# Optimization experiments

Measured on AMD Instinct MI355X. Metric: run time of the kernel, lower is better.

Reference implementation:

```python
import jax, jax.numpy as jnp
import numpy as np

B, CIN, COUT, N = 8, 64, 64, 4096
MODES, L, M = 64, 100, 20


def _cc_nodes_weights(m):
    # Clenshaw-Curtis nodes cos(k*pi/n) and weights on [-1, 1]
    n = m - 1
    k = np.arange(m)
    nodes = np.cos(np.pi * k / n)
    v = np.ones(m)
    for j in range(1, n // 2 + 1):
        b = 1.0 if 2 * j == n else 2.0
        v -= b / (4.0 * j * j - 1.0) * np.cos(2.0 * j * k * np.pi / n)
    w = 2.0 * v / n
    w[0] *= 0.5
    w[-1] *= 0.5
    return nodes, w


def setup_inputs() -> dict:
    key = jax.random.key(0)
    k1, k2, k3 = jax.random.split(key, 3)
    scale = 1.0 / (CIN * COUT)
    x = jax.random.normal(k1, (B, CIN, N), dtype=jnp.float32)
    w_real = scale * jax.random.uniform(k2, (CIN, COUT, MODES), dtype=jnp.float32)
    w_imag = scale * jax.random.uniform(k3, (CIN, COUT, MODES), dtype=jnp.float32)
    return {"x": x, "w_real": w_real, "w_imag": w_imag}


def _forward(x, w_real, w_imag):
    b, c, n = x.shape
    t = jnp.linspace(0.0, 1.0, n)
    f = np.fft.fftfreq(n, d=1.0 / n).astype(np.float32)  # integer freqs, fft order
    nodes, cw = _cc_nodes_weights(M)

    # ---- CFT: X(f) = sum_{segments l, cheb nodes k} w_lk * x(t_lk) * exp(-2i*pi*f*t_lk)
    h = 0.5 / L                               # segment half-width on [0,1]
    cents = (np.arange(L) + 0.5) / L
    t_nodes = (cents[:, None] + h * nodes[None, :]).ravel().astype(np.float32)  # (L*M,)
    wts = np.broadcast_to(h * cw, (L, M)).ravel().astype(np.float32)            # (L*M,)
    tq = jnp.asarray(t_nodes)
    # interpolate each (b, c) signal onto the Chebyshev quadrature nodes
    xs = jax.vmap(lambda s: jnp.interp(tq, t, s))(x.reshape(b * c, n))  # (BC, LM)
    phase = -2.0 * jnp.pi * jnp.asarray(f)[:, None] * tq[None, :]       # (N, LM)
    E = jnp.exp(1j * phase).astype(jnp.complex64) * jnp.asarray(wts)[None, :]
    x_cft = (xs.astype(jnp.complex64) @ E.T).reshape(b, c, n)           # (B, Cin, N)

    # ---- spectral channel mixing on lowest MODES fft-order frequencies
    w = (w_real + 1j * w_imag).astype(jnp.complex64)
    out_low = jnp.einsum('bix,iox->box', x_cft[:, :, :MODES], w)
    out_ft = jnp.concatenate(
        [out_low, jnp.zeros((b, COUT, n - MODES), dtype=jnp.complex64)], axis=-1)

    # ---- ICFT: x(t) = int X(f) exp(+2i*pi*f*t) df via the same segment quadrature
    order = np.argsort(f)
    f_sorted = f[order]
    cs = out_ft[:, :, jnp.asarray(order)].reshape(b * COUT, n)
    fa, fb = float(f_sorted[0]), float(f_sorted[-1])
    hf = (fb - fa) / (2.0 * L)
    fc = fa + (np.arange(L) + 0.5) * (fb - fa) / L
    f_nodes = (fc[:, None] + hf * nodes[None, :]).ravel().astype(np.float32)
    wfs = np.broadcast_to(hf * cw, (L, M)).ravel().astype(np.float32)
    fq = jnp.asarray(f_nodes)
    fs = jnp.asarray(f_sorted)
    ci = jax.vmap(lambda cv: jnp.interp(fq, fs, cv.real)
                  + 1j * jnp.interp(fq, fs, cv.imag))(cs)               # (BC, LM)
    phase2 = 2.0 * jnp.pi * fq[:, None] * t[None, :]                     # (LM, N)
    E2 = jnp.exp(1j * phase2).astype(jnp.complex64) * jnp.asarray(wfs)[:, None]
    return (ci.astype(jnp.complex64) @ E2).real.reshape(b, COUT, n)


def reference(x, w_real, w_imag):
    return _forward(x, w_real, w_imag)
```

## Files before the change

### kernel.cpp

```cpp
#include <hip/hip_runtime.h>


#define NN 4096
#define C1_19 0.9863613034027223
#define NS3 33
#define NSP 40

#define OFF_XRE 0
#define OFF_XIM 32768
#define OFF_Z   131072

__device__ __forceinline__ float sin_rev(float r) { return __builtin_amdgcn_sinf(r); }
__device__ __forceinline__ float cos_rev(float r) { return __builtin_amdgcn_cosf(r); }

__device__ __forceinline__ void build_tables(double* nd, double* cwd, int t) {
    if (t == 0) {
        nd[0] = 1.0; nd[1] = C1_19;
        for (int k = 2; k < 20; ++k) nd[k] = 2.0 * C1_19 * nd[k - 1] - nd[k - 2];
    }
    __syncthreads();
    if (t < 20) {
        double v = 1.0;
        for (int j = 1; j <= 9; ++j) {
            int q = (2 * j * t) % 38; if (q > 19) q = 38 - q;
            v -= 2.0 / (4.0 * j * j - 1.0) * nd[q];
        }
        double w = 2.0 * v / 19.0;
        if (t == 0 || t == 19) w *= 0.5;
        cwd[t] = w;
    }
}

__global__ __launch_bounds__(256) void k_cft(const float* __restrict__ x,
                                             float* __restrict__ ws) {
    __shared__ double nd[20], cwd[20];
    __shared__ __align__(16) float xs[2052];
    __shared__ __align__(16) float xq[1000];
    __shared__ __align__(16) float Fri[20][64][2];
    __shared__ float red[4][64][2];
    const int t = threadIdx.x;
    const int bc = blockIdx.x, h = blockIdx.y;
    const int i0 = h ? 2044 : 0;
    build_tables(nd, cwd, t);
    for (int idx = t; idx < 513; idx += 256)
        *(float4*)&xs[idx * 4] = *(const float4*)&x[(size_t)bc * NN + i0 + idx * 4];
    __syncthreads();
    for (int idx = t; idx < 1280; idx += 256) {
        int k = idx >> 6, m = idx & 63;
        double r = -0.005 * nd[k] * (double)m;
        r -= floor(r);
        float fr = (float)r;
        float w = (float)(0.005 * cwd[k]);
        Fri[k][m][0] = w * cos_rev(fr);
        Fri[k][m][1] = w * sin_rev(fr);
    }
    for (int idx = t; idx < 1000; idx += 256) {
        int l_loc = idx / 20, k = idx - l_loc * 20;
        int l = h * 50 + l_loc;
        double tq = 0.005 * ((double)(2 * l + 1) + nd[k]);
        double sf = tq * 4095.0;
        int i = (int)sf; if (i > 4094) i = 4094;
        double a = sf - (double)i;
        if (a < 0.0) a = 0.0; if (a > 1.0) a = 1.0;
        float af = (float)a;
        xq[idx] = (1.f - af) * xs[i - i0] + af * xs[i - i0 + 1];
    }
    __syncthreads();
    const int m = t & 63, grp = t >> 6;
    float Fre[20], Fim[20];
#pragma unroll
    for (int k = 0; k < 20; ++k) {
        Fre[k] = Fri[k][m][0];
        Fim[k] = Fri[k][m][1];
    }
    float ar = 0.f, ai = 0.f;
    for (int l_loc = grp; l_loc < 50; l_loc += 4) {
        const float4* q4 = (const float4*)&xq[l_loc * 20];
        float ur = 0.f, ui = 0.f;
#pragma unroll
        for (int c = 0; c < 5; ++c) {
            float4 q = q4[c];
            ur += q.x * Fre[c * 4]     + q.y * Fre[c * 4 + 1]
                + q.z * Fre[c * 4 + 2] + q.w * Fre[c * 4 + 3];
            ui += q.x * Fim[c * 4]     + q.y * Fim[c * 4 + 1]
                + q.z * Fim[c * 4 + 2] + q.w * Fim[c * 4 + 3];
        }
        int l = h * 50 + l_loc;
        int u = (m * (2 * l + 1)) % 200;
        float fr = (float)u * 0.005f;
        float tr = cos_rev(fr), ti = -sin_rev(fr);
        ar += tr * ur - ti * ui;
        ai += tr * ui + ti * ur;
    }
    red[grp][m][0] = ar;
    red[grp][m][1] = ai;
    __syncthreads();
    if (t < 64) {
        float sr = (red[0][t][0] + red[1][t][0]) + (red[2][t][0] + red[3][t][0]);
        float si = (red[0][t][1] + red[1][t][1]) + (red[2][t][1] + red[3][t][1]);
        const int base = h * 65536;
        ws[base + OFF_XRE + (size_t)bc * 64 + t] = sr;
        ws[base + OFF_XIM + (size_t)bc * 64 + t] = si;
    }
}

__global__ __launch_bounds__(256) void k_mix(const float* __restrict__ wr,
                                             const float* __restrict__ wi,
                                             float* __restrict__ ws) {
    __shared__ double nd[20], cwd[20];
    __shared__ float part[4][2][64];
    __shared__ float yt[2][64];
    __shared__ float sw0[NS3], sw1[NS3];
    __shared__ int   si0[NS3], si1[NS3];
    const int t = threadIdx.x;
    const int b = blockIdx.x >> 6, o = blockIdx.x & 63;
    build_tables(nd, cwd, t);
    __syncthreads();
    if (t < NS3) {
        int l = (t < 2) ? 49 : (t < 22 ? 50 : 51);
        int k = (t < 2) ? t : (t < 22 ? t - 2 : t - 13);
        double fq = -2048.0 + ((double)l + 0.5) * 40.95 + 20.475 * nd[k];
        int m0 = (int)floor(fq);
        float fr = (float)(fq - (double)m0);
        sw0[t] = (m0 >= 0 && m0 <= 63) ? (1.f - fr) : 0.f;
        sw1[t] = (m0 + 1 >= 0 && m0 + 1 <= 63) ? fr : 0.f;
        si0[t] = min(max(m0, 0), 63);
        si1[t] = min(max(m0 + 1, 0), 63);
    }
    const int m = t & 63, grp = t >> 6;
    float yr = 0.f, yi = 0.f;
#pragma unroll 4
    for (int i = grp * 16; i < grp * 16 + 16; ++i) {
        const size_t off = (size_t)(b * 64 + i) * 64 + m;
        float xr = ws[OFF_XRE + off] + ws[65536 + OFF_XRE + off];
        float xi = ws[OFF_XIM + off] + ws[65536 + OFF_XIM + off];
        float a = wr[((size_t)i * 64 + o) * 64 + m];
        float c = wi[((size_t)i * 64 + o) * 64 + m];
        yr += xr * a - xi * c;
        yi += xr * c + xi * a;
    }
    part[grp][0][m] = yr;
    part[grp][1][m] = yi;
    __syncthreads();
    if (t < 128) {
        int pr = t >> 6, mm = t & 63;
        yt[pr][mm] = ((part[0][pr][mm] + part[1][pr][mm]) +
                      (part[2][pr][mm] + part[3][pr][mm]));
    }
    __syncthreads();
    if (t < 2 * NS3) {
        int p = t >= NS3, s = t - p * NS3;
        float z = sw0[s] * yt[p][si0[s]] + sw1[s] * yt[p][si1[s]];
        ws[OFF_Z + (size_t)p * 512 * NSP + ((size_t)b * 64 + o) * NSP + s] = z;
    } else if (t < 2 * NS3 + 14) {
        int q = t - 2 * NS3;
        int p = q / 7, s = NS3 + q % 7;
        ws[OFF_Z + (size_t)p * 512 * NSP + ((size_t)b * 64 + o) * NSP + s] = 0.f;
    }
}

__global__ __launch_bounds__(256) void k_icft(const float* __restrict__ ws,
                                              float* __restrict__ out) {
    __shared__ double nd[20], cwd[20];
    __shared__ double sfq[NS3];
    __shared__ float  swf[NS3];
    __shared__ __align__(16) float zt[2][64][41];
    __shared__ __align__(16) float e2[2][NSP][36];
    const int t = threadIdx.x;
    const int jt2 = blockIdx.x, pc = blockIdx.y;
    build_tables(nd, cwd, t);
    __syncthreads();
    if (t < NS3) {
        int l = (t < 2) ? 49 : (t < 22 ? 50 : 51);
        int k = (t < 2) ? t : (t < 22 ? t - 2 : t - 13);
        sfq[t] = -2048.0 + ((double)l + 0.5) * 40.95 + 20.475 * nd[k];
        swf[t] = (float)(20.475 * cwd[k]);
    }
    for (int idx = t; idx < 2 * 64 * NSP; idx += 256) {
        int part = idx / (64 * NSP), rem = idx % (64 * NSP);
        int row = rem / NSP, s = rem % NSP;
        zt[part][row][s] =
            ws[OFF_Z + (size_t)part * 512 * NSP + ((size_t)pc * 64 + row) * NSP + s];
    }
    __syncthreads();
    const double inv4095 = 1.0 / 4095.0;
    for (int idx = t; idx < NSP * 32; idx += 256) {
        int s = idx >> 5, jl = idx & 31;
        float cr = 0.f, ci = 0.f;
        if (s < NS3) {
            double ph = sfq[s] * ((double)(jt2 * 32 + jl) * inv4095);
            ph -= floor(ph);
            float fr = (float)ph;
            cr = swf[s] * cos_rev(fr);
            ci = swf[s] * sin_rev(fr);
        }
        e2[0][s][jl + (jl >> 3) * 0] = cr;
        e2[1][s][jl] = ci;
        e2[0][s][jl] = cr;
    }
    __syncthreads();
    const int jg = t & 7, pg = t >> 3;
    float acc[2][4] = {{0.f}};
    for (int s0 = 0; s0 < NSP; s0 += 8) {
        float zr[2][8], zi[2][8];
#pragma unroll
        for (int p = 0; p < 2; ++p)
#pragma unroll
            for (int v = 0; v < 8; ++v) {
                zr[p][v] = zt[0][pg * 2 + p][s0 + v];
                zi[p][v] = zt[1][pg * 2 + p][s0 + v];
            }
#pragma unroll
        for (int v = 0; v < 8; ++v) {
            const float4 er = *(const float4*)&e2[0][s0 + v][jg * 4];
            const float4 ei = *(const float4*)&e2[1][s0 + v][jg * 4];
#pragma unroll
            for (int p = 0; p < 2; ++p) {
                acc[p][0] += zr[p][v] * er.x - zi[p][v] * ei.x;
                acc[p][1] += zr[p][v] * er.y - zi[p][v] * ei.y;
                acc[p][2] += zr[p][v] * er.z - zi[p][v] * ei.z;
                acc[p][3] += zr[p][v] * er.w - zi[p][v] * ei.w;
            }
        }
    }
#pragma unroll
    for (int p = 0; p < 2; ++p) {
        float4 r;
        r.x = acc[p][0]; r.y = acc[p][1]; r.z = acc[p][2]; r.w = acc[p][3];
        *(float4*)&out[(size_t)(pc * 64 + pg * 2 + p) * NN + jt2 * 32 + jg * 4] = r;
    }
}

extern "C" void kernel_launch(void* const* d_in, const int* in_sizes, int n_in,
                              void* d_out, int out_size, void* d_ws, size_t ws_size,
                              hipStream_t stream) {
    const float* x  = (const float*)d_in[0];
    const float* wr = (const float*)d_in[1];
    const float* wi = (const float*)d_in[2];
    float* out = (float*)d_out;
    float* ws  = (float*)d_ws;
    (void)in_sizes; (void)n_in; (void)out_size; (void)ws_size;

    k_cft<<<dim3(512, 2), 256, 0, stream>>>(x, ws);
    k_mix<<<512, 256, 0, stream>>>(wr, wi, ws);
    k_icft<<<dim3(128, 8), 256, 0, stream>>>(ws, out);
}
```

Measured before the change: 31.17 us.

## Fuse CFT and mode-mixing kernels using flag-based inter-block dependency

Merges the CFT and channel-mixing launches into one grid. The first 512 blocks each compute a full signal's CFT, with no split into halves. The remaining 512 blocks stage the weight slices in shared memory and spin-wait on per-row magic flags written into the output buffer before mixing. This removes one kernel launch, the half-split partial-sum round trip, and some strided global weight reads. In exchange it relies on producer blocks being scheduled before or alongside consumers to avoid deadlock, and it temporarily uses the output buffer as flag storage.

```diff
diff --git a/kernel.cpp b/kernel.cpp
--- a/kernel.cpp
+++ b/kernel.cpp
@@ -5,10 +5,11 @@
 #define C1_19 0.9863613034027223
 #define NS3 33
 #define NSP 40
+#define MAGIC 0x7fc0deadu
 
 #define OFF_XRE 0
 #define OFF_XIM 32768
-#define OFF_Z   131072
+#define OFF_Z   65536
 
 __device__ __forceinline__ float sin_rev(float r) { return __builtin_amdgcn_sinf(r); }
 __device__ __forceinline__ float cos_rev(float r) { return __builtin_amdgcn_cosf(r); }
@@ -31,131 +32,157 @@
     }
 }
 
-__global__ __launch_bounds__(256) void k_cft(const float* __restrict__ x,
-                                             float* __restrict__ ws) {
+struct PA { float xs[NN]; float xq[2000]; float Fri[20][64][2]; float red[4][64][2]; };
+struct PB { float wsl[2][64][64]; float part[4][2][64]; float yt[2][64]; };
+union SU { PA a; PB b; };
+
+__global__ __launch_bounds__(256, 4) void k_cftmix(const float* __restrict__ x,
+                                                   const float* __restrict__ wr,
+                                                   const float* __restrict__ wi,
+                                                   float* __restrict__ ws,
+                                                   float* __restrict__ out) {
+    __shared__ SU su;
     __shared__ double nd[20], cwd[20];
-    __shared__ __align__(16) float xs[2052];
-    __shared__ __align__(16) float xq[1000];
-    __shared__ __align__(16) float Fri[20][64][2];
-    __shared__ float red[4][64][2];
-    const int t = threadIdx.x;
-    const int bc = blockIdx.x, h = blockIdx.y;
-    const int i0 = h ? 2044 : 0;
-    build_tables(nd, cwd, t);
-    for (int idx = t; idx < 513; idx += 256)
-        *(float4*)&xs[idx * 4] = *(const float4*)&x[(size_t)bc * NN + i0 + idx * 4];
-    __syncthreads();
-    for (int idx = t; idx < 1280; idx += 256) {
-        int k = idx >> 6, m = idx & 63;
-        double r = -0.005 * nd[k] * (double)m;
-        r -= floor(r);
-        float fr = (float)r;
-        float w = (float)(0.005 * cwd[k]);
-        Fri[k][m][0] = w * cos_rev(fr);
-        Fri[k][m][1] = w * sin_rev(fr);
-    }
-    for (int idx = t; idx < 1000; idx += 256) {
-        int l_loc = idx / 20, k = idx - l_loc * 20;
-        int l = h * 50 + l_loc;
-        double tq = 0.005 * ((double)(2 * l + 1) + nd[k]);
-        double sf = tq * 4095.0;
-        int i = (int)sf; if (i > 4094) i = 4094;
-        double a = sf - (double)i;
-        if (a < 0.0) a = 0.0; if (a > 1.0) a = 1.0;
-        float af = (float)a;
-        xq[idx] = (1.f - af) * xs[i - i0] + af * xs[i - i0 + 1];
-    }
-    __syncthreads();
-    const int m = t & 63, grp = t >> 6;
-    float Fre[20], Fim[20];
-#pragma unroll
-    for (int k = 0; k < 20; ++k) {
-        Fre[k] = Fri[k][m][0];
-        Fim[k] = Fri[k][m][1];
-    }
-    float ar = 0.f, ai = 0.f;
-    for (int l_loc = grp; l_loc < 50; l_loc += 4) {
-        const float4* q4 = (const float4*)&xq[l_loc * 20];
-        float ur = 0.f, ui = 0.f;
-#pragma unroll
-        for (int c = 0; c < 5; ++c) {
-            float4 q = q4[c];
-            ur += q.x * Fre[c * 4]     + q.y * Fre[c * 4 + 1]
-                + q.z * Fre[c * 4 + 2] + q.w * Fre[c * 4 + 3];
-            ui += q.x * Fim[c * 4]     + q.y * Fim[c * 4 + 1]
-                + q.z * Fim[c * 4 + 2] + q.w * Fim[c * 4 + 3];
-        }
-        int l = h * 50 + l_loc;
-        int u = (m * (2 * l + 1)) % 200;
-        float fr = (float)u * 0.005f;
-        float tr = cos_rev(fr), ti = -sin_rev(fr);
-        ar += tr * ur - ti * ui;
-        ai += tr * ui + ti * ur;
-    }
-    red[grp][m][0] = ar;
-    red[grp][m][1] = ai;
-    __syncthreads();
-    if (t < 64) {
-        float sr = (red[0][t][0] + red[1][t][0]) + (red[2][t][0] + red[3][t][0]);
-        float si = (red[0][t][1] + red[1][t][1]) + (red[2][t][1] + red[3][t][1]);
-        const int base = h * 65536;
-        ws[base + OFF_XRE + (size_t)bc * 64 + t] = sr;
-        ws[base + OFF_XIM + (size_t)bc * 64 + t] = si;
-    }
-}
-
-__global__ __launch_bounds__(256) void k_mix(const float* __restrict__ wr,
-                                             const float* __restrict__ wi,
-                                             float* __restrict__ ws) {
-    __shared__ double nd[20], cwd[20];
-    __shared__ float part[4][2][64];
-    __shared__ float yt[2][64];
     __shared__ float sw0[NS3], sw1[NS3];
     __shared__ int   si0[NS3], si1[NS3];
     const int t = threadIdx.x;
-    const int b = blockIdx.x >> 6, o = blockIdx.x & 63;
-    build_tables(nd, cwd, t);
-    __syncthreads();
-    if (t < NS3) {
-        int l = (t < 2) ? 49 : (t < 22 ? 50 : 51);
-        int k = (t < 2) ? t : (t < 22 ? t - 2 : t - 13);
-        double fq = -2048.0 + ((double)l + 0.5) * 40.95 + 20.475 * nd[k];
-        int m0 = (int)floor(fq);
-        float fr = (float)(fq - (double)m0);
-        sw0[t] = (m0 >= 0 && m0 <= 63) ? (1.f - fr) : 0.f;
-        sw1[t] = (m0 + 1 >= 0 && m0 + 1 <= 63) ? fr : 0.f;
-        si0[t] = min(max(m0, 0), 63);
-        si1[t] = min(max(m0 + 1, 0), 63);
-    }
-    const int m = t & 63, grp = t >> 6;
-    float yr = 0.f, yi = 0.f;
+    const int vb = blockIdx.x;
+
+    if (vb < 512) {
+        const int bc = vb;
+        build_tables(nd, cwd, t);
+#pragma unroll
+        for (int it = 0; it < 4; ++it) {
+            int c4 = it * 256 + t;
+            *(float4*)&su.a.xs[c4 * 4] = *(const float4*)&x[(size_t)bc * NN + c4 * 4];
+        }
+        __syncthreads();
+        for (int idx = t; idx < 1280; idx += 256) {
+            int k = idx >> 6, m = idx & 63;
+            double r = -0.005 * nd[k] * (double)m;
+            r -= floor(r);
+            float fr = (float)r;
+            float w = (float)(0.005 * cwd[k]);
+            su.a.Fri[k][m][0] = w * cos_rev(fr);
+            su.a.Fri[k][m][1] = w * sin_rev(fr);
+        }
+#pragma unroll
+        for (int it = 0; it < 8; ++it) {
+            int node = it * 256 + t;
+            if (node < 2000) {
+                int l = node / 20, k = node - l * 20;
+                double tq = 0.005 * ((double)(2 * l + 1) + nd[k]);
+                double sf = tq * 4095.0;
+                int i = (int)sf; if (i > 4094) i = 4094;
+                double a = sf - (double)i;
+                if (a < 0.0) a = 0.0; if (a > 1.0) a = 1.0;
+                float af = (float)a;
+                su.a.xq[node] = (1.f - af) * su.a.xs[i] + af * su.a.xs[i + 1];
+            }
+        }
+        __syncthreads();
+        const int m = t & 63, grp = t >> 6;
+        float Fre[20], Fim[20];
+#pragma unroll
+        for (int k = 0; k < 20; ++k) {
+            Fre[k] = su.a.Fri[k][m][0];
+            Fim[k] = su.a.Fri[k][m][1];
+        }
+        float ar = 0.f, ai = 0.f;
+        for (int l = grp * 25; l < grp * 25 + 25; ++l) {
+            const float4* q4 = (const float4*)&su.a.xq[l * 20];
+            float ur = 0.f, ui = 0.f;
+#pragma unroll
+            for (int c = 0; c < 5; ++c) {
+                float4 q = q4[c];
+                ur += q.x * Fre[c * 4]     + q.y * Fre[c * 4 + 1]
+                    + q.z * Fre[c * 4 + 2] + q.w * Fre[c * 4 + 3];
+                ui += q.x * Fim[c * 4]     + q.y * Fim[c * 4 + 1]
+                    + q.z * Fim[c * 4 + 2] + q.w * Fim[c * 4 + 3];
+            }
+            int u = (m * (2 * l + 1)) % 200;
+            float fr = (float)u * 0.005f;
+            float tr = cos_rev(fr), ti = -sin_rev(fr);
+            ar += tr * ur - ti * ui;
+            ai += tr * ui + ti * ur;
+        }
+        su.a.red[grp][m][0] = ar;
+        su.a.red[grp][m][1] = ai;
+        __syncthreads();
+        if (t < 64) {
+            float sr = (su.a.red[0][t][0] + su.a.red[1][t][0]) +
+                       (su.a.red[2][t][0] + su.a.red[3][t][0]);
+            float si = (su.a.red[0][t][1] + su.a.red[1][t][1]) +
+                       (su.a.red[2][t][1] + su.a.red[3][t][1]);
+            __hip_atomic_store(&ws[OFF_XRE + (size_t)bc * 64 + t], sr,
+                               __ATOMIC_RELAXED, __HIP_MEMORY_SCOPE_SYSTEM);
+            __hip_atomic_store(&ws[OFF_XIM + (size_t)bc * 64 + t], si,
+                               __ATOMIC_RELAXED, __HIP_MEMORY_SCOPE_SYSTEM);
+        }
+        __syncthreads();
+        if (t == 0)
+            __hip_atomic_store((unsigned*)out + (size_t)bc * 16, MAGIC,
+                               __ATOMIC_RELAXED, __HIP_MEMORY_SCOPE_SYSTEM);
+    } else {
+        const int id = vb - 512;
+        const int b = id >> 6, o = id & 63;
+        build_tables(nd, cwd, t);
+        __syncthreads();
+        if (t < NS3) {
+            int l = (t < 2) ? 49 : (t < 22 ? 50 : 51);
+            int k = (t < 2) ? t : (t < 22 ? t - 2 : t - 13);
+            double fq = -2048.0 + ((double)l + 0.5) * 40.95 + 20.475 * nd[k];
+            int m0 = (int)floor(fq);
+            float fr = (float)(fq - (double)m0);
+            sw0[t] = (m0 >= 0 && m0 <= 63) ? (1.f - fr) : 0.f;
+            sw1[t] = (m0 + 1 >= 0 && m0 + 1 <= 63) ? fr : 0.f;
+            si0[t] = min(max(m0, 0), 63);
+            si1[t] = min(max(m0 + 1, 0), 63);
+        }
+        for (int idx = t; idx < 2048; idx += 256) {
+            int arr = idx >> 10, rem = idx & 1023;
+            int i = rem >> 4, c4 = rem & 15;
+            const float* src = arr ? wi : wr;
+            *(float4*)&su.b.wsl[arr][i][c4 * 4] =
+                *(const float4*)&src[(((size_t)i * 64 + o) << 6) + c4 * 4];
+        }
+        if (t < 64) {
+            const unsigned* fp = (const unsigned*)out + (size_t)(b * 64 + t) * 16;
+            while (__hip_atomic_load(fp, __ATOMIC_RELAXED,
+                                     __HIP_MEMORY_SCOPE_SYSTEM) != MAGIC)
+                __builtin_amdgcn_s_sleep(2);
+        }
+        __syncthreads();
+        const int m = t & 63, grp = t >> 6;
+        float yr = 0.f, yi = 0.f;
 #pragma unroll 4
-    for (int i = grp * 16; i < grp * 16 + 16; ++i) {
-        const size_t off = (size_t)(b * 64 + i) * 64 + m;
-        float xr = ws[OFF_XRE + off] + ws[65536 + OFF_XRE + off];
-        float xi = ws[OFF_XIM + off] + ws[65536 + OFF_XIM + off];
-        float a = wr[((size_t)i * 64 + o) * 64 + m];
-        float c = wi[((size_t)i * 64 + o) * 64 + m];
-        yr += xr * a - xi * c;
-        yi += xr * c + xi * a;
-    }
-    part[grp][0][m] = yr;
-    part[grp][1][m] = yi;
-    __syncthreads();
-    if (t < 128) {
-        int pr = t >> 6, mm = t & 63;
-        yt[pr][mm] = ((part[0][pr][mm] + part[1][pr][mm]) +
-                      (part[2][pr][mm] + part[3][pr][mm]));
-    }
-    __syncthreads();
-    if (t < 2 * NS3) {
-        int p = t >= NS3, s = t - p * NS3;
-        float z = sw0[s] * yt[p][si0[s]] + sw1[s] * yt[p][si1[s]];
-        ws[OFF_Z + (size_t)p * 512 * NSP + ((size_t)b * 64 + o) * NSP + s] = z;
-    } else if (t < 2 * NS3 + 14) {
-        int q = t - 2 * NS3;
-        int p = q / 7, s = NS3 + q % 7;
-        ws[OFF_Z + (size_t)p * 512 * NSP + ((size_t)b * 64 + o) * NSP + s] = 0.f;
+        for (int i = grp * 16; i < grp * 16 + 16; ++i) {
+            const size_t off = (size_t)(b * 64 + i) * 64 + m;
+            float xr = ws[OFF_XRE + off];
+            float xi = ws[OFF_XIM + off];
+            float a = su.b.wsl[0][i][m];
+            float c = su.b.wsl[1][i][m];
+            yr += xr * a - xi * c;
+            yi += xr * c + xi * a;
+        }
+        su.b.part[grp][0][m] = yr;
+        su.b.part[grp][1][m] = yi;
+        __syncthreads();
+        if (t < 128) {
+            int pr = t >> 6, mm = t & 63;
+            su.b.yt[pr][mm] = ((su.b.part[0][pr][mm] + su.b.part[1][pr][mm]) +
+                               (su.b.part[2][pr][mm] + su.b.part[3][pr][mm]));
+        }
+        __syncthreads();
+        if (t < 2 * NS3) {
+            int p = t >= NS3, s = t - p * NS3;
+            float z = sw0[s] * su.b.yt[p][si0[s]] + sw1[s] * su.b.yt[p][si1[s]];
+            ws[OFF_Z + (size_t)p * 512 * NSP + ((size_t)b * 64 + o) * NSP + s] = z;
+        } else if (t < 2 * NS3 + 14) {
+            int q = t - 2 * NS3;
+            int p = q / 7, s = NS3 + q % 7;
+            ws[OFF_Z + (size_t)p * 512 * NSP + ((size_t)b * 64 + o) * NSP + s] = 0.f;
+        }
     }
 }
 
@@ -194,9 +221,8 @@
             cr = swf[s] * cos_rev(fr);
             ci = swf[s] * sin_rev(fr);
         }
-        e2[0][s][jl + (jl >> 3) * 0] = cr;
+        e2[0][s][jl] = cr;
         e2[1][s][jl] = ci;
-        e2[0][s][jl] = cr;
     }
     __syncthreads();
     const int jg = t & 7, pg = t >> 3;
@@ -241,7 +267,6 @@
     float* ws  = (float*)d_ws;
     (void)in_sizes; (void)n_in; (void)out_size; (void)ws_size;
 
-    k_cft<<<dim3(512, 2), 256, 0, stream>>>(x, ws);
-    k_mix<<<512, 256, 0, stream>>>(wr, wi, ws);
+    k_cftmix<<<1024, 256, 0, stream>>>(x, wr, wi, ws, out);
     k_icft<<<dim3(128, 8), 256, 0, stream>>>(ws, out);
 }
```

Result: faster. 29.91 us, median of 2 (-4.0%).
